# Kernel tuning notes

Measured on AMD Instinct MI355X. Metric: run time of the kernel, lower is better.

## Reference

```python
import jax, jax.numpy as jnp
import numpy as np

N = 50000      # nodes
E = 800000     # edges (avg degree 16)
IN = 256       # input feature dim
H = 4          # heads
F = 64         # out_feats per head
EF = 64        # edge_feats
NT = 8         # num_etypes
SLOPE = 0.2    # leaky relu negative slope


def setup_inputs() -> dict:
    key = jax.random.key(0)
    ks = jax.random.split(key, 10)
    return {
        "nfeat": jax.random.normal(ks[0], (N, IN), dtype=jnp.float32),
        "fc_w": jax.random.normal(ks[1], (IN, H * F), dtype=jnp.float32) * 0.05,
        "fc_e_w": jax.random.normal(ks[2], (EF, H * EF), dtype=jnp.float32) * 0.05,
        "attn_l": jax.random.normal(ks[3], (H, F), dtype=jnp.float32) * 0.1,
        "attn_r": jax.random.normal(ks[4], (H, F), dtype=jnp.float32) * 0.1,
        "attn_e": jax.random.normal(ks[5], (H, EF), dtype=jnp.float32) * 0.1,
        "edge_emb": jax.random.normal(ks[6], (NT, EF), dtype=jnp.float32),
        "src": jax.random.randint(ks[7], (E,), 0, N, dtype=jnp.int32),
        "dst": jax.random.randint(ks[8], (E,), 0, N, dtype=jnp.int32),
        "etype": jax.random.randint(ks[9], (E,), 0, NT, dtype=jnp.int32),
    }


def reference(nfeat, fc_w, fc_e_w, attn_l, attn_r, attn_e, edge_emb, src, dst, etype):
    # node projection: [N, H, F]
    feat = (nfeat @ fc_w).reshape(N, H, F)
    # per-node attention halves: [N, H]
    el = jnp.einsum("nhf,hf->nh", feat, attn_l)
    er = jnp.einsum("nhf,hf->nh", feat, attn_r)
    # per-etype edge attention term: fc_e(edge_emb).view(NT,H,EF) . attn_e -> [NT, H]
    e_feat = (edge_emb @ fc_e_w).reshape(NT, H, EF)
    ee = jnp.einsum("the,he->th", e_feat, attn_e)
    # raw edge scores: [E, H]
    e = el[src] + er[dst] + ee[etype]
    a_raw = jax.nn.leaky_relu(e, negative_slope=SLOPE)
    # edge_softmax over destination nodes (homogeneous graph -> all edges together)
    seg_max = jax.ops.segment_max(a_raw, dst, num_segments=N)  # [N, H]
    a_exp = jnp.exp(a_raw - seg_max[dst])
    seg_sum = jax.ops.segment_sum(a_exp, dst, num_segments=N)  # [N, H]
    a = a_exp / seg_sum[dst]                                   # [E, H]
    # weighted gather-sum aggregation: sum_e a[e] * feat[src[e]] per dst
    msg = feat[src] * a[:, :, None]                            # [E, H, F]
    rst = jax.ops.segment_sum(msg, dst, num_segments=N)        # [N, H, F]
    return rst, a
```

## Files before the change

### kernel.cpp

```cpp
#include <hip/hip_runtime.h>

#define N_NODES 50000
#define E_EDGES 800000
#define IN_DIM 256
#define H_HEADS 4
#define F_OUT 64
#define EF_DIM 64
#define NT_TYPES 8
#define SLOPE 0.2f
#define HF 256

typedef __attribute__((ext_vector_type(8))) short short8;
typedef __attribute__((ext_vector_type(4))) float f32x4;
typedef unsigned short ushort_t;
typedef unsigned long long u64;

#define FEATBF_OFF 0
#define EL_OFF   6400000
#define ER_OFF   6600000
#define EE_OFF   6800000
#define BT_OFF   6800064
#define INT_OFF  6832832
#define DEG_IOFF     0
#define CURSOR_IOFF  50000
#define RL_IOFF      100000
#define PK_IOFF      150008
#define BO_IOFF      1750008

#define NBLK_GEMM 782
#define NBLK_E4   782
#define NCHUNK    196

__device__ __forceinline__ ushort_t f2bf(float f) {
    unsigned u = __float_as_uint(f);
    u += 0x7fffu + ((u >> 16) & 1u);
    return (ushort_t)(u >> 16);
}
__device__ __forceinline__ float bf2f(ushort_t b) {
    return __uint_as_float(((unsigned)b) << 16);
}

__global__ __launch_bounds__(256) void k1_prep(
    const float* __restrict__ edge_emb, const float* __restrict__ fc_e_w,
    const float* __restrict__ attn_e, const float* __restrict__ fc_w,
    float* __restrict__ ee, ushort_t* __restrict__ Bt,
    const int* __restrict__ dst, int* __restrict__ deg)
{
    const int b = blockIdx.x;
    if (b == 0) {
        const int c = threadIdx.x;
        const float ae = attn_e[c];
        const int lane = c & 63, h = c >> 6;
        for (int ty = 0; ty < NT_TYPES; ty++) {
            float v = 0.f;
            #pragma unroll 8
            for (int k = 0; k < EF_DIM; k++)
                v = fmaf(edge_emb[ty * EF_DIM + k], fc_e_w[k * (H_HEADS * EF_DIM) + c], v);
            float contrib = v * ae;
            #pragma unroll
            for (int m = 32; m >= 1; m >>= 1) contrib += __shfl_xor(contrib, m);
            if (lane == 0) ee[ty * H_HEADS + h] = contrib;
        }
    } else if (b <= 256) {
        const int k = b - 1, c = threadIdx.x;
        Bt[(size_t)c * 256 + k] = f2bf(fc_w[(size_t)k * 256 + c]);
    } else {
        const int t = (b - 257) * 256 + threadIdx.x;
        if (t < E_EDGES / 4) {
            const int4 d4 = ((const int4*)dst)[t];
            atomicAdd(deg + d4.x, 1);
            atomicAdd(deg + d4.y, 1);
            atomicAdd(deg + d4.z, 1);
            atomicAdd(deg + d4.w, 1);
        }
    }
}

__global__ __launch_bounds__(256) void scanA(
    const int* __restrict__ deg, int* __restrict__ rl, int* __restrict__ bo)
{
    __shared__ int sm[256];
    const int c = blockIdx.x, t = threadIdx.x;
    const int g = c * 256 + t;
    const int v = (g < N_NODES) ? deg[g] : 0;
    sm[t] = v;
    __syncthreads();
    int val = v;
    #pragma unroll
    for (int o = 1; o < 256; o <<= 1) {
        int x = (t >= o) ? sm[t - o] : 0;
        __syncthreads();
        val += x;
        sm[t] = val;
        __syncthreads();
    }
    if (g < N_NODES) rl[g] = val - v;
    if (t == 255) bo[c] = val;
}

__global__ __launch_bounds__(256) void scanB(int* __restrict__ bo)
{
    __shared__ int sm[256];
    const int t = threadIdx.x;
    const int v = (t < NCHUNK) ? bo[t] : 0;
    sm[t] = v;
    __syncthreads();
    int val = v;
    #pragma unroll
    for (int o = 1; o < 256; o <<= 1) {
        int x = (t >= o) ? sm[t - o] : 0;
        __syncthreads();
        val += x;
        sm[t] = val;
        __syncthreads();
    }
    if (t < NCHUNK) bo[t] = val - v;
}

__device__ __forceinline__ void gemm_body(
    const float* __restrict__ nfeat, const ushort_t* __restrict__ Bt,
    const float* __restrict__ attn_l, const float* __restrict__ attn_r,
    ushort_t* __restrict__ feat, float* __restrict__ el, float* __restrict__ er,
    int blk)
{
    const int w    = threadIdx.x >> 6;
    const int lane = threadIdx.x & 63;
    const int n16  = lane & 15;
    const int quad = lane >> 4;
    const int row0 = blk * 64;

    f32x4 acc[4][4];
    #pragma unroll
    for (int rt = 0; rt < 4; rt++)
        #pragma unroll
        for (int ct = 0; ct < 4; ct++)
            acc[rt][ct] = (f32x4){0.f, 0.f, 0.f, 0.f};

    for (int kb = 0; kb < IN_DIM; kb += 32) {
        short8 a[4], b[4];
        #pragma unroll
        for (int rt = 0; rt < 4; rt++) {
            int r = row0 + rt * 16 + n16;
            r = r < N_NODES ? r : N_NODES - 1;
            const float* p = nfeat + (size_t)r * IN_DIM + kb + quad * 8;
            const float4 v0 = *(const float4*)p;
            const float4 v1 = *(const float4*)(p + 4);
            short8 t;
            t[0] = (short)f2bf(v0.x); t[1] = (short)f2bf(v0.y);
            t[2] = (short)f2bf(v0.z); t[3] = (short)f2bf(v0.w);
            t[4] = (short)f2bf(v1.x); t[5] = (short)f2bf(v1.y);
            t[6] = (short)f2bf(v1.z); t[7] = (short)f2bf(v1.w);
            a[rt] = t;
        }
        #pragma unroll
        for (int ct = 0; ct < 4; ct++) {
            const int c = w * 64 + ct * 16 + n16;
            b[ct] = *(const short8*)(Bt + (size_t)c * 256 + kb + quad * 8);
        }
        #pragma unroll
        for (int rt = 0; rt < 4; rt++)
            #pragma unroll
            for (int ct = 0; ct < 4; ct++)
                acc[rt][ct] = __builtin_amdgcn_mfma_f32_16x16x32_bf16(a[rt], b[ct], acc[rt][ct], 0, 0, 0);
    }

    float alv[4], arv[4];
    #pragma unroll
    for (int ct = 0; ct < 4; ct++) {
        alv[ct] = attn_l[w * 64 + ct * 16 + n16];
        arv[ct] = attn_r[w * 64 + ct * 16 + n16];
    }
    #pragma unroll
    for (int rt = 0; rt < 4; rt++) {
        #pragma unroll
        for (int reg = 0; reg < 4; reg++) {
            const int row = row0 + rt * 16 + quad * 4 + reg;
            const bool ok = row < N_NODES;
            float pl = 0.f, pr = 0.f;
            #pragma unroll
            for (int ct = 0; ct < 4; ct++) {
                const float v = acc[rt][ct][reg];
                if (ok) feat[(size_t)row * HF + w * 64 + ct * 16 + n16] = f2bf(v);
                pl = fmaf(v, alv[ct], pl);
                pr = fmaf(v, arv[ct], pr);
            }
            #pragma unroll
            for (int m = 8; m >= 1; m >>= 1) {
                pl += __shfl_xor(pl, m);
                pr += __shfl_xor(pr, m);
            }
            if (n16 == 0 && ok) {
                el[row * H_HEADS + w] = pl;
                er[row * H_HEADS + w] = pr;
            }
        }
    }
}

__global__ __launch_bounds__(256) void k3_gemm_scatter(
    const float* __restrict__ nfeat, const ushort_t* __restrict__ Bt,
    const float* __restrict__ attn_l, const float* __restrict__ attn_r,
    ushort_t* __restrict__ feat, float* __restrict__ el, float* __restrict__ er,
    const int* __restrict__ src, const int* __restrict__ dst, const int* __restrict__ etype,
    const int* __restrict__ rl, const int* __restrict__ bo,
    int* __restrict__ cursor, u64* __restrict__ pk)
{
    if (blockIdx.x < NBLK_GEMM) {
        gemm_body(nfeat, Bt, attn_l, attn_r, feat, el, er, blockIdx.x);
    } else {
        const int t = ((int)blockIdx.x - NBLK_GEMM) * 256 + threadIdx.x;
        if (t < E_EDGES / 4) {
            const int4 s4 = ((const int4*)src)[t];
            const int4 d4 = ((const int4*)dst)[t];
            const int4 e4 = ((const int4*)etype)[t];
            const int eb = t * 4;
            int pos;
            pos = bo[d4.x >> 8] + rl[d4.x] + atomicAdd(cursor + d4.x, 1);
            pk[pos] = (u64)s4.x | ((u64)e4.x << 16) | ((u64)(eb + 0) << 32);
            pos = bo[d4.y >> 8] + rl[d4.y] + atomicAdd(cursor + d4.y, 1);
            pk[pos] = (u64)s4.y | ((u64)e4.y << 16) | ((u64)(eb + 1) << 32);
            pos = bo[d4.z >> 8] + rl[d4.z] + atomicAdd(cursor + d4.z, 1);
            pk[pos] = (u64)s4.z | ((u64)e4.z << 16) | ((u64)(eb + 2) << 32);
            pos = bo[d4.w >> 8] + rl[d4.w] + atomicAdd(cursor + d4.w, 1);
            pk[pos] = (u64)s4.w | ((u64)e4.w << 16) | ((u64)(eb + 3) << 32);
        }
    }
}

__device__ void agg_fallback(
    int d, int off, int deg, int h, int l,
    const u64* __restrict__ pk, const float* __restrict__ el,
    const float erh, const float* __restrict__ ee,
    const uint2* __restrict__ fb, float* __restrict__ a_out, float* __restrict__ rst)
{
    float m = -INFINITY;
    for (int i = l; i < deg; i += 16) {
        const u64 p = pk[off + i];
        float v = el[(int)(p & 0xffffu) * 4 + h] + erh + ee[(int)((p >> 16) & 0xffu) * 4 + h];
        v = v > 0.f ? v : SLOPE * v;
        m = fmaxf(m, v);
    }
    m = fmaxf(m, __shfl_xor(m, 1));
    m = fmaxf(m, __shfl_xor(m, 2));
    m = fmaxf(m, __shfl_xor(m, 4));
    m = fmaxf(m, __shfl_xor(m, 8));
    float s = 0.f;
    for (int i = l; i < deg; i += 16) {
        const u64 p = pk[off + i];
        float v = el[(int)(p & 0xffffu) * 4 + h] + erh + ee[(int)((p >> 16) & 0xffu) * 4 + h];
        v = v > 0.f ? v : SLOPE * v;
        s += __expf(v - m);
    }
    s += __shfl_xor(s, 1);
    s += __shfl_xor(s, 2);
    s += __shfl_xor(s, 4);
    s += __shfl_xor(s, 8);
    const float inv = 1.f / s;
    for (int i = l; i < deg; i += 16) {
        const u64 p = pk[off + i];
        const int sn = (int)(p & 0xffffu);
        float v = el[sn * 4 + h] + erh + ee[(int)((p >> 16) & 0xffu) * 4 + h];
        v = v > 0.f ? v : SLOPE * v;
        a_out[(int)(p >> 32) * 4 + h] = __expf(v - m) * inv;
    }
    float4 acc = {0.f, 0.f, 0.f, 0.f};
    const int col = h * 16 + l;
    for (int e = 0; e < deg; e++) {
        const u64 p = pk[off + e];
        const int sn = (int)(p & 0xffffu);
        float v = el[sn * 4 + h] + erh + ee[(int)((p >> 16) & 0xffu) * 4 + h];
        v = v > 0.f ? v : SLOPE * v;
        const float aw = __expf(v - m) * inv;
        const uint2 u = fb[(size_t)sn * 64 + col];
        acc.x = fmaf(aw, __uint_as_float(u.x << 16),         acc.x);
        acc.y = fmaf(aw, __uint_as_float(u.x & 0xffff0000u), acc.y);
        acc.z = fmaf(aw, __uint_as_float(u.y << 16),         acc.z);
        acc.w = fmaf(aw, __uint_as_float(u.y & 0xffff0000u), acc.w);
    }
    *(float4*)(rst + (size_t)d * HF + h * 64 + l * 4) = acc;
}

__global__ __launch_bounds__(256) void agg_kernel(
    const u64* __restrict__ pk, const int* __restrict__ rl, const int* __restrict__ bo,
    const int* __restrict__ degarr,
    const float* __restrict__ el, const float* __restrict__ er,
    const float* __restrict__ ee, const ushort_t* __restrict__ feat,
    float* __restrict__ a_out, float* __restrict__ rst)
{
    const int wid  = threadIdx.x >> 6;
    const int lane = threadIdx.x & 63;
    const int h    = lane >> 4;
    const int l    = lane & 15;
    const int dA   = blockIdx.x * 8 + wid * 2;
    const int dB   = dA + 1;

    __shared__ __align__(16) float    sExp[4][2][256];
    __shared__ __align__(16) ushort_t sSrc[4][2][64];

    float* expA = sExp[wid][0];
    float* expB = sExp[wid][1];
    ushort_t* srcA = sSrc[wid][0];
    ushort_t* srcB = sSrc[wid][1];
    const uint2* fb = (const uint2*)feat;

    const int offA = bo[dA >> 8] + rl[dA];
    const int offB = bo[dB >> 8] + rl[dB];
    const int degA = degarr[dA];
    const int degB = degarr[dB];
    const float erhA = er[dA * 4 + h];
    const float erhB = er[dB * 4 + h];
    const bool fsA = (degA <= 64);
    const bool fsB = (degB <= 64);
    const int nchA = fsA ? (degA + 15) >> 4 : 0;
    const int nchB = fsB ? (degB + 15) >> 4 : 0;
    const int ncm  = nchA > nchB ? nchA : nchB;

    float mA = -INFINITY, mB = -INFINITY;
    for (int c = 0; c < ncm; c++) {
        const int e = c * 16 + l;
        const bool inA = (c < nchA);
        const bool inB = (c < nchB);
        const bool ldA = inA && (e < degA);
        const bool ldB = inB && (e < degB);
        u64 pA = 0, pB = 0;
        if (ldA) pA = pk[offA + e];
        if (ldB) pB = pk[offB + e];
        if (inA) {
            float v = -INFINITY;
            if (ldA) {
                const int s  = (int)(pA & 0xffffu);
                const int ty = (int)((pA >> 16) & 0xffu);
                if (h == 0) srcA[e] = (ushort_t)s;
                v = el[s * 4 + h] + erhA + ee[ty * 4 + h];
                v = v > 0.f ? v : SLOPE * v;
                expA[e * 4 + h] = v;
            } else if (h == 0) srcA[e] = 0;
            mA = fmaxf(mA, v);
        }
        if (inB) {
            float v = -INFINITY;
            if (ldB) {
                const int s  = (int)(pB & 0xffffu);
                const int ty = (int)((pB >> 16) & 0xffu);
                if (h == 0) srcB[e] = (ushort_t)s;
                v = el[s * 4 + h] + erhB + ee[ty * 4 + h];
                v = v > 0.f ? v : SLOPE * v;
                expB[e * 4 + h] = v;
            } else if (h == 0) srcB[e] = 0;
            mB = fmaxf(mB, v);
        }
    }
    #pragma unroll
    for (int o = 8; o >= 1; o >>= 1) {
        mA = fmaxf(mA, __shfl_xor(mA, o));
        mB = fmaxf(mB, __shfl_xor(mB, o));
    }

    float sA = 0.f, sB = 0.f;
    for (int c = 0; c < nchA; c++) {
        const int e = c * 16 + l;
        float ev = 0.f;
        if (e < degA) ev = __expf(expA[e * 4 + h] - mA);
        expA[e * 4 + h] = ev;
        sA += ev;
    }
    for (int c = 0; c < nchB; c++) {
        const int e = c * 16 + l;
        float ev = 0.f;
        if (e < degB) ev = __expf(expB[e * 4 + h] - mB);
        expB[e * 4 + h] = ev;
        sB += ev;
    }
    #pragma unroll
    for (int o = 8; o >= 1; o >>= 1) {
        sA += __shfl_xor(sA, o);
        sB += __shfl_xor(sB, o);
    }
    const float invA = (degA > 0) ? 1.f / sA : 0.f;
    const float invB = (degB > 0) ? 1.f / sB : 0.f;

    asm volatile("s_waitcnt lgkmcnt(0)" ::: "memory");

    const float iA0 = __shfl(invA, 0),  iA1 = __shfl(invA, 16);
    const float iA2 = __shfl(invA, 32), iA3 = __shfl(invA, 48);
    const float iB0 = __shfl(invB, 0),  iB1 = __shfl(invB, 16);
    const float iB2 = __shfl(invB, 32), iB3 = __shfl(invB, 48);

    if (h == 0) {
        for (int c = 0; c < nchA; c++) {
            const int e = c * 16 + l;
            if (e < degA) {
                const int eid = (int)(pk[offA + e] >> 32);
                const float4 t = *(const float4*)(expA + e * 4);
                float4 av;
                av.x = t.x * iA0; av.y = t.y * iA1; av.z = t.z * iA2; av.w = t.w * iA3;
                *(float4*)(a_out + (size_t)eid * 4) = av;
            }
        }
    } else if (h == 1) {
        for (int c = 0; c < nchB; c++) {
            const int e = c * 16 + l;
            if (e < degB) {
                const int eid = (int)(pk[offB + e] >> 32);
                const float4 t = *(const float4*)(expB + e * 4);
                float4 av;
                av.x = t.x * iB0; av.y = t.y * iB1; av.z = t.z * iB2; av.w = t.w * iB3;
                *(float4*)(a_out + (size_t)eid * 4) = av;
            }
        }
    }

    const int degPA = nchA << 4;
    const int degPB = nchB << 4;
    const int degPm = degPA > degPB ? degPA : degPB;
    const int col = h * 16 + l;
    float4 accA = {0.f, 0.f, 0.f, 0.f};
    float4 accB = {0.f, 0.f, 0.f, 0.f};
    for (int e0 = 0; e0 < degPm; e0 += 8) {
        const bool gA = e0 < degPA;
        const bool gB = e0 < degPB;
        uint2 uA[8], uB[8];
        float wA[8], wB[8];
        if (gA) {
            #pragma unroll
            for (int j = 0; j < 8; j++) {
                const int e = e0 + j;
                wA[j] = expA[e * 4 + h];
                uA[j] = fb[(size_t)srcA[e] * 64 + col];
            }
        }
        if (gB) {
            #pragma unroll
            for (int j = 0; j < 8; j++) {
                const int e = e0 + j;
                wB[j] = expB[e * 4 + h];
                uB[j] = fb[(size_t)srcB[e] * 64 + col];
            }
        }
        if (gA) {
            #pragma unroll
            for (int j = 0; j < 8; j++) {
                accA.x = fmaf(wA[j], __uint_as_float(uA[j].x << 16),         accA.x);
                accA.y = fmaf(wA[j], __uint_as_float(uA[j].x & 0xffff0000u), accA.y);
                accA.z = fmaf(wA[j], __uint_as_float(uA[j].y << 16),         accA.z);
                accA.w = fmaf(wA[j], __uint_as_float(uA[j].y & 0xffff0000u), accA.w);
            }
        }
        if (gB) {
            #pragma unroll
            for (int j = 0; j < 8; j++) {
                accB.x = fmaf(wB[j], __uint_as_float(uB[j].x << 16),         accB.x);
                accB.y = fmaf(wB[j], __uint_as_float(uB[j].x & 0xffff0000u), accB.y);
                accB.z = fmaf(wB[j], __uint_as_float(uB[j].y << 16),         accB.z);
                accB.w = fmaf(wB[j], __uint_as_float(uB[j].y & 0xffff0000u), accB.w);
            }
        }
    }
    if (fsA) {
        accA.x *= invA; accA.y *= invA; accA.z *= invA; accA.w *= invA;
        *(float4*)(rst + (size_t)dA * HF + h * 64 + l * 4) = accA;
    }
    if (fsB) {
        accB.x *= invB; accB.y *= invB; accB.z *= invB; accB.w *= invB;
        *(float4*)(rst + (size_t)dB * HF + h * 64 + l * 4) = accB;
    }
    if (!fsA) agg_fallback(dA, offA, degA, h, l, pk, el, erhA, ee, fb, a_out, rst);
    if (!fsB) agg_fallback(dB, offB, degB, h, l, pk, el, erhB, ee, fb, a_out, rst);
}

extern "C" void kernel_launch(void* const* d_in, const int* in_sizes, int n_in,
                              void* d_out, int out_size, void* d_ws, size_t ws_size,
                              hipStream_t stream) {
    const float* nfeat    = (const float*)d_in[0];
    const float* fc_w     = (const float*)d_in[1];
    const float* fc_e_w   = (const float*)d_in[2];
    const float* attn_l   = (const float*)d_in[3];
    const float* attn_r   = (const float*)d_in[4];
    const float* attn_e   = (const float*)d_in[5];
    const float* edge_emb = (const float*)d_in[6];
    const int*   src      = (const int*)d_in[7];
    const int*   dst      = (const int*)d_in[8];
    const int*   etype    = (const int*)d_in[9];

    float* ws = (float*)d_ws;
    ushort_t* feat = (ushort_t*)(ws + FEATBF_OFF);
    float* el   = ws + EL_OFF;
    float* er   = ws + ER_OFF;
    float* ee   = ws + EE_OFF;
    ushort_t* Bt = (ushort_t*)(ws + BT_OFF);
    int*   ip      = (int*)(ws + INT_OFF);
    int*   deg     = ip + DEG_IOFF;
    int*   cursor  = ip + CURSOR_IOFF;
    int*   rl      = ip + RL_IOFF;
    u64*   pk      = (u64*)(ip + PK_IOFF);
    int*   bo      = ip + BO_IOFF;

    float* rst   = (float*)d_out;
    float* a_out = (float*)d_out + (size_t)N_NODES * HF;

    hipMemsetAsync(deg, 0, 2 * N_NODES * sizeof(int), stream);
    k1_prep<<<1039, 256, 0, stream>>>(edge_emb, fc_e_w, attn_e, fc_w, ee, Bt, dst, deg);
    scanA<<<NCHUNK, 256, 0, stream>>>(deg, rl, bo);
    scanB<<<1, 256, 0, stream>>>(bo);
    k3_gemm_scatter<<<NBLK_GEMM + NBLK_E4, 256, 0, stream>>>(
        nfeat, Bt, attn_l, attn_r, feat, el, er,
        src, dst, etype, rl, bo, cursor, pk);
    agg_kernel<<<N_NODES / 8, 256, 0, stream>>>(
        pk, rl, bo, deg, el, er, ee, feat, a_out, rst);
}
```

Baseline: 313.9 us.

## Record per-edge rank during degree counting, padding counters to separate cache lines

The degree-count atomic now returns each edge's rank within its destination, stored as a 16-bit value. A separate placement kernel then writes the CSR entries with no second atomic pass or cursor array. Degree counters are padded to 16 ints apart so that concurrent atomics on different nodes do not share a cache line. The degree counting also moves into the GEMM launch, which adds an extra placement kernel launch and a 16x larger memset and counter array.

```diff
diff --git a/kernel.cpp b/kernel.cpp
--- a/kernel.cpp
+++ b/kernel.cpp
@@ -21,13 +21,14 @@
 #define EE_OFF   6800000
 #define BT_OFF   6800064
 #define INT_OFF  6832832
-#define DEG_IOFF     0
-#define CURSOR_IOFF  50000
-#define RL_IOFF      100000
-#define PK_IOFF      150008
-#define BO_IOFF      1750008
+#define DEGP_IOFF    0
+#define RL_IOFF      800000
+#define BO_IOFF      850000
+#define RANK_IOFF    850256
+#define PK_IOFF      1250256
 
 #define NBLK_GEMM 782
+#define NBLK_E1   3125
 #define NBLK_E4   782
 #define NCHUNK    196
 
@@ -43,8 +44,7 @@
 __global__ __launch_bounds__(256) void k1_prep(
     const float* __restrict__ edge_emb, const float* __restrict__ fc_e_w,
     const float* __restrict__ attn_e, const float* __restrict__ fc_w,
-    float* __restrict__ ee, ushort_t* __restrict__ Bt,
-    const int* __restrict__ dst, int* __restrict__ deg)
+    float* __restrict__ ee, ushort_t* __restrict__ Bt)
 {
     const int b = blockIdx.x;
     if (b == 0) {
@@ -61,60 +61,10 @@
             for (int m = 32; m >= 1; m >>= 1) contrib += __shfl_xor(contrib, m);
             if (lane == 0) ee[ty * H_HEADS + h] = contrib;
         }
-    } else if (b <= 256) {
+    } else {
         const int k = b - 1, c = threadIdx.x;
         Bt[(size_t)c * 256 + k] = f2bf(fc_w[(size_t)k * 256 + c]);
-    } else {
-        const int t = (b - 257) * 256 + threadIdx.x;
-        if (t < E_EDGES / 4) {
-            const int4 d4 = ((const int4*)dst)[t];
-            atomicAdd(deg + d4.x, 1);
-            atomicAdd(deg + d4.y, 1);
-            atomicAdd(deg + d4.z, 1);
-            atomicAdd(deg + d4.w, 1);
-        }
-    }
-}
-
-__global__ __launch_bounds__(256) void scanA(
-    const int* __restrict__ deg, int* __restrict__ rl, int* __restrict__ bo)
-{
-    __shared__ int sm[256];
-    const int c = blockIdx.x, t = threadIdx.x;
-    const int g = c * 256 + t;
-    const int v = (g < N_NODES) ? deg[g] : 0;
-    sm[t] = v;
-    __syncthreads();
-    int val = v;
-    #pragma unroll
-    for (int o = 1; o < 256; o <<= 1) {
-        int x = (t >= o) ? sm[t - o] : 0;
-        __syncthreads();
-        val += x;
-        sm[t] = val;
-        __syncthreads();
-    }
-    if (g < N_NODES) rl[g] = val - v;
-    if (t == 255) bo[c] = val;
-}
-
-__global__ __launch_bounds__(256) void scanB(int* __restrict__ bo)
-{
-    __shared__ int sm[256];
-    const int t = threadIdx.x;
-    const int v = (t < NCHUNK) ? bo[t] : 0;
-    sm[t] = v;
-    __syncthreads();
-    int val = v;
-    #pragma unroll
-    for (int o = 1; o < 256; o <<= 1) {
-        int x = (t >= o) ? sm[t - o] : 0;
-        __syncthreads();
-        val += x;
-        sm[t] = val;
-        __syncthreads();
-    }
-    if (t < NCHUNK) bo[t] = val - v;
+    }
 }
 
 __device__ __forceinline__ void gemm_body(
@@ -197,34 +147,83 @@
     }
 }
 
-__global__ __launch_bounds__(256) void k3_gemm_scatter(
+__global__ __launch_bounds__(256) void k2_gemm_rank(
     const float* __restrict__ nfeat, const ushort_t* __restrict__ Bt,
     const float* __restrict__ attn_l, const float* __restrict__ attn_r,
     ushort_t* __restrict__ feat, float* __restrict__ el, float* __restrict__ er,
-    const int* __restrict__ src, const int* __restrict__ dst, const int* __restrict__ etype,
-    const int* __restrict__ rl, const int* __restrict__ bo,
-    int* __restrict__ cursor, u64* __restrict__ pk)
+    const int* __restrict__ dst, int* __restrict__ degp, ushort_t* __restrict__ rank)
 {
     if (blockIdx.x < NBLK_GEMM) {
         gemm_body(nfeat, Bt, attn_l, attn_r, feat, el, er, blockIdx.x);
     } else {
-        const int t = ((int)blockIdx.x - NBLK_GEMM) * 256 + threadIdx.x;
-        if (t < E_EDGES / 4) {
-            const int4 s4 = ((const int4*)src)[t];
-            const int4 d4 = ((const int4*)dst)[t];
-            const int4 e4 = ((const int4*)etype)[t];
-            const int eb = t * 4;
-            int pos;
-            pos = bo[d4.x >> 8] + rl[d4.x] + atomicAdd(cursor + d4.x, 1);
-            pk[pos] = (u64)s4.x | ((u64)e4.x << 16) | ((u64)(eb + 0) << 32);
-            pos = bo[d4.y >> 8] + rl[d4.y] + atomicAdd(cursor + d4.y, 1);
-            pk[pos] = (u64)s4.y | ((u64)e4.y << 16) | ((u64)(eb + 1) << 32);
-            pos = bo[d4.z >> 8] + rl[d4.z] + atomicAdd(cursor + d4.z, 1);
-            pk[pos] = (u64)s4.z | ((u64)e4.z << 16) | ((u64)(eb + 2) << 32);
-            pos = bo[d4.w >> 8] + rl[d4.w] + atomicAdd(cursor + d4.w, 1);
-            pk[pos] = (u64)s4.w | ((u64)e4.w << 16) | ((u64)(eb + 3) << 32);
-        }
-    }
+        const int e = ((int)blockIdx.x - NBLK_GEMM) * 256 + threadIdx.x;
+        const int d = dst[e];
+        rank[e] = (ushort_t)atomicAdd(degp + (d << 4), 1);
+    }
+}
+
+__global__ __launch_bounds__(256) void scanA(
+    const int* __restrict__ degp, int* __restrict__ rl, int* __restrict__ bo)
+{
+    __shared__ int sm[256];
+    const int c = blockIdx.x, t = threadIdx.x;
+    const int g = c * 256 + t;
+    const int v = (g < N_NODES) ? degp[g << 4] : 0;
+    sm[t] = v;
+    __syncthreads();
+    int val = v;
+    #pragma unroll
+    for (int o = 1; o < 256; o <<= 1) {
+        int x = (t >= o) ? sm[t - o] : 0;
+        __syncthreads();
+        val += x;
+        sm[t] = val;
+        __syncthreads();
+    }
+    if (g < N_NODES) rl[g] = val - v;
+    if (t == 255) bo[c] = val;
+}
+
+__global__ __launch_bounds__(256) void scanB(int* __restrict__ bo)
+{
+    __shared__ int sm[256];
+    const int t = threadIdx.x;
+    const int v = (t < NCHUNK) ? bo[t] : 0;
+    sm[t] = v;
+    __syncthreads();
+    int val = v;
+    #pragma unroll
+    for (int o = 1; o < 256; o <<= 1) {
+        int x = (t >= o) ? sm[t - o] : 0;
+        __syncthreads();
+        val += x;
+        sm[t] = val;
+        __syncthreads();
+    }
+    if (t < NCHUNK) bo[t] = val - v;
+}
+
+__global__ __launch_bounds__(256) void k4_place(
+    const int* __restrict__ src, const int* __restrict__ dst, const int* __restrict__ etype,
+    const ushort_t* __restrict__ rank,
+    const int* __restrict__ rl, const int* __restrict__ bo, u64* __restrict__ pk)
+{
+    const int t = blockIdx.x * 256 + threadIdx.x;
+    if (t >= E_EDGES / 4) return;
+    const int4 s4 = ((const int4*)src)[t];
+    const int4 d4 = ((const int4*)dst)[t];
+    const int4 e4 = ((const int4*)etype)[t];
+    const ushort4 r4 = ((const ushort4*)rank)[t];
+    const int eb = t * 4;
+    int pos;
+    pos = bo[d4.x >> 8] + rl[d4.x] + (int)r4.x;
+    pk[pos] = (u64)s4.x | ((u64)e4.x << 16) | ((u64)(eb + 0) << 32);
+    pos = bo[d4.y >> 8] + rl[d4.y] + (int)r4.y;
+    pk[pos] = (u64)s4.y | ((u64)e4.y << 16) | ((u64)(eb + 1) << 32);
+    pos = bo[d4.z >> 8] + rl[d4.z] + (int)r4.z;
+    pk[pos] = (u64)s4.z | ((u64)e4.z << 16) | ((u64)(eb + 2) << 32);
+    pos = bo[d4.w >> 8] + rl[d4.w] + (int)r4.w;
+    pk[pos] = (u64)s4.w | ((u64)e4.w << 16) | ((u64)(eb + 3) << 32);
 }
 
 __device__ void agg_fallback(
@@ -282,7 +281,7 @@
 
 __global__ __launch_bounds__(256) void agg_kernel(
     const u64* __restrict__ pk, const int* __restrict__ rl, const int* __restrict__ bo,
-    const int* __restrict__ degarr,
+    const int* __restrict__ degp,
     const float* __restrict__ el, const float* __restrict__ er,
     const float* __restrict__ ee, const ushort_t* __restrict__ feat,
     float* __restrict__ a_out, float* __restrict__ rst)
@@ -305,8 +304,8 @@
 
     const int offA = bo[dA >> 8] + rl[dA];
     const int offB = bo[dB >> 8] + rl[dB];
-    const int degA = degarr[dA];
-    const int degB = degarr[dB];
+    const int degA = degp[dA << 4];
+    const int degB = degp[dB << 4];
     const float erhA = er[dA * 4 + h];
     const float erhB = er[dB * 4 + h];
     const bool fsA = (degA <= 64);
@@ -489,22 +488,22 @@
     float* ee   = ws + EE_OFF;
     ushort_t* Bt = (ushort_t*)(ws + BT_OFF);
     int*   ip      = (int*)(ws + INT_OFF);
-    int*   deg     = ip + DEG_IOFF;
-    int*   cursor  = ip + CURSOR_IOFF;
+    int*   degp    = ip + DEGP_IOFF;
     int*   rl      = ip + RL_IOFF;
+    int*   bo      = ip + BO_IOFF;
+    ushort_t* rank = (ushort_t*)(ip + RANK_IOFF);
     u64*   pk      = (u64*)(ip + PK_IOFF);
-    int*   bo      = ip + BO_IOFF;
 
     float* rst   = (float*)d_out;
     float* a_out = (float*)d_out + (size_t)N_NODES * HF;
 
-    hipMemsetAsync(deg, 0, 2 * N_NODES * sizeof(int), stream);
-    k1_prep<<<1039, 256, 0, stream>>>(edge_emb, fc_e_w, attn_e, fc_w, ee, Bt, dst, deg);
-    scanA<<<NCHUNK, 256, 0, stream>>>(deg, rl, bo);
+    hipMemsetAsync(degp, 0, (size_t)N_NODES * 16 * sizeof(int), stream);
+    k1_prep<<<257, 256, 0, stream>>>(edge_emb, fc_e_w, attn_e, fc_w, ee, Bt);
+    k2_gemm_rank<<<NBLK_GEMM + NBLK_E1, 256, 0, stream>>>(
+        nfeat, Bt, attn_l, attn_r, feat, el, er, dst, degp, rank);
+    scanA<<<NCHUNK, 256, 0, stream>>>(degp, rl, bo);
     scanB<<<1, 256, 0, stream>>>(bo);
-    k3_gemm_scatter<<<NBLK_GEMM + NBLK_E4, 256, 0, stream>>>(
-        nfeat, Bt, attn_l, attn_r, feat, el, er,
-        src, dst, etype, rl, bo, cursor, pk);
+    k4_place<<<NBLK_E4, 256, 0, stream>>>(src, dst, etype, rank, rl, bo, pk);
     agg_kernel<<<N_NODES / 8, 256, 0, stream>>>(
-        pk, rl, bo, deg, el, er, ee, feat, a_out, rst);
-}
+        pk, rl, bo, degp, el, er, ee, feat, a_out, rst);
+}
```

New measurement: 298.3 us. 5.0% less time.
